# Optimization experiments

Measured on AMD Instinct MI355X. Metric: run time of the kernel, lower is better.

Reference implementation:

```python
import jax, jax.numpy as jnp
import numpy as np

H = 2048      # hidden_size
I = 768       # moe_intermediate_size
E = 32        # num_experts
K = 8         # num_experts_per_tok (top_k)
T = 1024      # tokens (batch * seq)


def setup_inputs() -> dict:
    key = jax.random.key(0)
    k1, k2, k3, k4 = jax.random.split(key, 4)
    return {
        "hidden_states": jax.random.normal(k1, (T, H), jnp.float32),
        "gate_weight": jax.random.normal(k2, (E, H), jnp.float32) * 0.02,
        "w13_weight": jax.random.normal(k3, (E, 2 * I, H), jnp.float32) * 0.02,
        "w2_weight": jax.random.normal(k4, (E, H, I), jnp.float32) * 0.02,
    }


def reference(hidden_states, gate_weight, w13_weight, w2_weight):
    x = hidden_states  # [T, H]
    # --- router (Qwen3MoeSparseMoeBlock gating) ---
    logits = x @ gate_weight.T                      # [T, E]
    probs = jax.nn.softmax(logits, axis=-1)
    topk_w, topk_idx = jax.lax.top_k(probs, K)      # [T, K]
    topk_w = topk_w / jnp.sum(topk_w, axis=-1, keepdims=True)  # norm_topk_prob
    # dense combine matrix [T, E]: routing weight per (token, expert), 0 if not selected
    combine = jnp.zeros((x.shape[0], E), x.dtype).at[
        jnp.arange(x.shape[0])[:, None], topk_idx
    ].add(topk_w)
    # --- expert FFNs (fused gate+up = w13, SiLU-gated, then w2 down-proj) ---
    h = jnp.einsum('th,eoh->eto', x, w13_weight)    # [E, T, 2I]
    gate, up = h[:, :, :I], h[:, :, I:]
    act = jax.nn.silu(gate) * up                    # [E, T, I]
    y = jnp.einsum('eti,ehi->eth', act, w2_weight)  # [E, T, H]
    # --- weighted combine ---
    return jnp.einsum('eth,te->th', y, combine)     # [T, H]
```

## Files before the change

kernel.cpp:

```cpp
#include <hip/hip_runtime.h>
#include <hip/hip_bf16.h>
#include <math.h>

#define T_TOK 1024
#define H_DIM 2048
#define I_DIM 768
#define E_NUM 32
#define K_TOP 8
#define BK 32
#define GRID_P 1024

typedef __bf16 bf16x8 __attribute__((ext_vector_type(8)));
typedef float  f32x4  __attribute__((ext_vector_type(4)));

__device__ __forceinline__ bf16x8 cvt2_bf16(const f32x4 a, const f32x4 b) {
    bf16x8 r;
    r[0] = (__bf16)a[0]; r[1] = (__bf16)a[1]; r[2] = (__bf16)a[2]; r[3] = (__bf16)a[3];
    r[4] = (__bf16)b[0]; r[5] = (__bf16)b[1]; r[6] = (__bf16)b[2]; r[7] = (__bf16)b[3];
    return r;
}

__device__ __forceinline__ int frag_off(int r, int kgrp8) {
    return (r >> 4) * 512 + kgrp8 * 128 + (r & 15) * 8;
}

__global__ __launch_bounds__(256) void router_kernel(
    const float* __restrict__ x, const float* __restrict__ gw,
    float* __restrict__ wdense, unsigned int* __restrict__ masks,
    __bf16* __restrict__ xb)
{
    const int t = blockIdx.x;
    const int tid = threadIdx.x;
    __shared__ float part[256];
    __shared__ float logits[E_NUM];

    {
        const float* xr2 = x + (size_t)t * H_DIM + tid * 8;
        const f32x4 a = *(const f32x4*)(xr2);
        const f32x4 b = *(const f32x4*)(xr2 + 4);
        *(bf16x8*)(xb + (size_t)t * H_DIM + tid * 8) = cvt2_bf16(a, b);
    }

    const int e = tid & 31;
    const int chunk = tid >> 5;
    const float* xr = x + (size_t)t * H_DIM;
    const float* gr = gw + (size_t)e * H_DIM;
    const int base = chunk * (H_DIM / 8);
    float s = 0.f;
    for (int h = 0; h < H_DIM / 8; h += 4) {
        const f32x4 xv = *reinterpret_cast<const f32x4*>(xr + base + h);
        const f32x4 gv = *reinterpret_cast<const f32x4*>(gr + base + h);
        s += xv[0]*gv[0] + xv[1]*gv[1] + xv[2]*gv[2] + xv[3]*gv[3];
    }
    part[tid] = s;
    __syncthreads();
    if (tid < E_NUM) {
        float tot = 0.f;
        for (int c = 0; c < 8; ++c) tot += part[c * 32 + tid];
        logits[tid] = tot;
    }
    __syncthreads();
    if (tid == 0) {
        float l[E_NUM];
        for (int i = 0; i < E_NUM; ++i) {
            l[i] = logits[i];
            wdense[(size_t)t * E_NUM + i] = 0.f;
        }
        unsigned mask = 0;
        int   idx[K_TOP];
        float lv[K_TOP];
        for (int k = 0; k < K_TOP; ++k) {
            float best = -1e30f; int bi = 0;
            for (int i = 0; i < E_NUM; ++i)
                if (!((mask >> i) & 1u) && l[i] > best) { best = l[i]; bi = i; }
            mask |= (1u << bi); idx[k] = bi; lv[k] = best;
        }
        const float m = lv[0];
        float den = 0.f;
        for (int k = 0; k < K_TOP; ++k) den += expf(lv[k] - m);
        for (int k = 0; k < K_TOP; ++k)
            wdense[(size_t)t * E_NUM + idx[k]] = expf(lv[k] - m) / den;
        masks[t] = mask;
    }
}

__global__ __launch_bounds__(1024) void route_kernel(
    const unsigned int* __restrict__ masks, const float* __restrict__ wdense,
    int* __restrict__ cnt, int* __restrict__ off, int* __restrict__ tbl,
    int* __restrict__ tok, float* __restrict__ wgt, int* __restrict__ posl)
{
    const int tid  = threadIdx.x;
    const int wv   = tid >> 6;
    const int lane = tid & 63;
    __shared__ int wcnt[E_NUM][16];
    __shared__ int woff[E_NUM][16];
    __shared__ int eoff[E_NUM];
    __shared__ int ecnt[E_NUM];

    const unsigned int m = masks[tid];
#pragma unroll
    for (int e = 0; e < E_NUM; ++e) {
        const unsigned long long b = __ballot((m >> e) & 1u);
        if (lane == 0) wcnt[e][wv] = __popcll(b);
    }
    __syncthreads();
    if (tid < E_NUM) {
        int r = 0;
        for (int w = 0; w < 16; ++w) { woff[tid][w] = r; r += wcnt[tid][w]; }
        ecnt[tid] = r;
    }
    __syncthreads();
    if (tid == 0) {
        int r = 0, nt = 0;
        for (int e = 0; e < E_NUM; ++e) {
            eoff[e] = r; off[e] = r;
            const int c = ecnt[e];
            cnt[e] = c;
            r += c;
            const int nz = (c + 127) >> 7;
            for (int z = 0; z < nz; ++z) tbl[1 + nt++] = (e << 8) | z;
        }
        tbl[0] = nt;
    }
    __syncthreads();
#pragma unroll
    for (int e = 0; e < E_NUM; ++e) {
        const int bit = (m >> e) & 1u;
        const unsigned long long b = __ballot(bit);
        if (bit) {
            const int pos = eoff[e] + woff[e][wv]
                          + (int)__popcll(b & ((1ULL << lane) - 1ULL));
            tok[pos] = tid;
            wgt[pos] = wdense[(size_t)tid * E_NUM + e];
            const int slot = __popc(m & ((1u << e) - 1u));
            posl[tid * K_TOP + slot] = pos;
        }
    }
}

#define GEMM_PHASE(P, Q)                                                       \
  {                                                                            \
    if (scur + 2 < NS) {                                                       \
      const int kk = (scur + 2) * BK;                                          \
      pa##P##_0 = *(const bf16x8*)(ap + kk);                                   \
      pa##P##_1 = *(const bf16x8*)(ap + kk + 8);                               \
      pb##P##_0 = *(const f32x4*)(wp + kk);                                    \
      pb##P##_1 = *(const f32x4*)(wp + kk + 4);                                \
      pb##P##_2 = *(const f32x4*)(wp + kk + 8);                                \
      pb##P##_3 = *(const f32x4*)(wp + kk + 12);                               \
    }                                                                          \
    bf16x8 af[4], bfr[4];                                                      \
    _Pragma("unroll")                                                          \
    for (int m = 0; m < 4; ++m)                                                \
      af[m] = *(const bf16x8*)&As[P][((wm >> 4) + m) * 512 + lane * 8];        \
    _Pragma("unroll")                                                          \
    for (int n = 0; n < 4; ++n)                                                \
      bfr[n] = *(const bf16x8*)&Bs[P][(wn * 4 + n) * 512 + lane * 8];          \
    __builtin_amdgcn_s_setprio(1);                                             \
    _Pragma("unroll")                                                          \
    for (int m = 0; m < 4; ++m)                                                \
      _Pragma("unroll")                                                        \
      for (int n = 0; n < 4; ++n)                                              \
        acc[m][n] = __builtin_amdgcn_mfma_f32_16x16x32_bf16(af[m], bfr[n],     \
                                                            acc[m][n], 0,0,0); \
    __builtin_amdgcn_s_setprio(0);                                             \
    if (scur + 1 < NS) {                                                       \
      *(bf16x8*)&As[Q][wo]       = pa##Q##_0;                                  \
      *(bf16x8*)&As[Q][wo + 128] = pa##Q##_1;                                  \
      *(bf16x8*)&Bs[Q][wo]       = cvt2_bf16(pb##Q##_0, pb##Q##_1);            \
      *(bf16x8*)&Bs[Q][wo + 128] = cvt2_bf16(pb##Q##_2, pb##Q##_3);            \
    }                                                                          \
    asm volatile("s_waitcnt lgkmcnt(0)" ::: "memory");                         \
    __builtin_amdgcn_s_barrier();                                              \
    ++scur;                                                                    \
  }

#define GEMM_PROLOGUE()                                                        \
    pa0_0 = *(const bf16x8*)(ap);                                              \
    pa0_1 = *(const bf16x8*)(ap + 8);                                          \
    pb0_0 = *(const f32x4*)(wp);                                               \
    pb0_1 = *(const f32x4*)(wp + 4);                                           \
    pb0_2 = *(const f32x4*)(wp + 8);                                           \
    pb0_3 = *(const f32x4*)(wp + 12);                                          \
    pa1_0 = *(const bf16x8*)(ap + BK);                                         \
    pa1_1 = *(const bf16x8*)(ap + BK + 8);                                     \
    pb1_0 = *(const f32x4*)(wp + BK);                                          \
    pb1_1 = *(const f32x4*)(wp + BK + 4);                                      \
    pb1_2 = *(const f32x4*)(wp + BK + 8);                                      \
    pb1_3 = *(const f32x4*)(wp + BK + 12);                                     \
    *(bf16x8*)&As[0][wo]       = pa0_0;                                        \
    *(bf16x8*)&As[0][wo + 128] = pa0_1;                                        \
    *(bf16x8*)&Bs[0][wo]       = cvt2_bf16(pb0_0, pb0_1);                      \
    *(bf16x8*)&Bs[0][wo + 128] = cvt2_bf16(pb0_2, pb0_3);                      \
    asm volatile("s_waitcnt lgkmcnt(0)" ::: "memory");                         \
    __builtin_amdgcn_s_barrier();

__global__ __launch_bounds__(256, 3) void gemm1_kernel(
    const __bf16* __restrict__ xb, const float* __restrict__ w13,
    const int* __restrict__ tok, const int* __restrict__ cnt,
    const int* __restrict__ off, const int* __restrict__ tbl,
    unsigned short* __restrict__ act)
{
    __shared__ __bf16 As[2][4096];
    __shared__ __bf16 Bs[2][4096];
    const int tid  = threadIdx.x;
    const int wid  = tid >> 6;
    const int lane = tid & 63;
    const int wm = (wid >> 1) * 64;
    const int wn = (wid & 1);
    const int lrow = lane & 15;
    const int sr = tid >> 1;
    const int kh = tid & 1;
    const int wo = frag_off(sr, kh * 2);
    const int NS = H_DIM / BK;

    const int W = tbl[0] * 12;
    for (int w = blockIdx.x; w < W; w += gridDim.x) {
        const int ti   = w / 12;
        const int nidx = w - ti * 12;
        const int ez = tbl[1 + ti];
        const int e  = ez >> 8;
        const int m0 = (ez & 255) * 128;
        const int c  = cnt[e];
        const int o  = off[e];
        const int n0 = nidx * 64;

        int rA = m0 + sr; rA = rA < c ? rA : c - 1;
        const __bf16* ap = xb + (size_t)tok[o + rA] * H_DIM + kh * 16;
        const int grp = sr >> 5;
        const int wrow = (grp & 1) * I_DIM + n0 + (grp >> 1) * 32 + (sr & 31);
        const float* wp = w13 + (size_t)e * (2 * I_DIM) * H_DIM
                              + (size_t)wrow * H_DIM + kh * 16;

        bf16x8 pa0_0, pa0_1, pa1_0, pa1_1;
        f32x4  pb0_0, pb0_1, pb0_2, pb0_3, pb1_0, pb1_1, pb1_2, pb1_3;
        f32x4  acc[4][4] = {};

        GEMM_PROLOGUE()

        int scur = 0;
        for (int it = 0; it < NS; it += 2) {
            GEMM_PHASE(0, 1)
            GEMM_PHASE(1, 0)
        }

#pragma unroll
        for (int m = 0; m < 4; ++m)
#pragma unroll
            for (int n = 0; n < 2; ++n)
#pragma unroll
                for (int i = 0; i < 4; ++i) {
                    const int row = m0 + wm + m * 16 + (lane >> 4) * 4 + i;
                    if (row < c) {
                        const int icol = n0 + wn * 32 + n * 16 + lrow;
                        const float g = acc[m][n][i];
                        const float u = acc[m][n + 2][i];
                        const float a = (g / (1.f + expf(-g))) * u;
                        act[(size_t)(o + row) * I_DIM + icol] =
                            __builtin_bit_cast(unsigned short, (__bf16)a);
                    }
                }
    }
}

__global__ __launch_bounds__(256, 3) void gemm2_kernel(
    const unsigned short* __restrict__ act, const float* __restrict__ w2,
    const int* __restrict__ tok, const float* __restrict__ wgt,
    const int* __restrict__ cnt, const int* __restrict__ off,
    const int* __restrict__ tbl, unsigned short* __restrict__ ybuf)
{
    __shared__ __bf16 As[2][4096];
    __shared__ __bf16 Bs[2][4096];
    const int tid  = threadIdx.x;
    const int wid  = tid >> 6;
    const int lane = tid & 63;
    const int wm = (wid >> 1) * 64;
    const int wn = (wid & 1);
    const int lrow = lane & 15;
    const int sr = tid >> 1;
    const int kh = tid & 1;
    const int wo = frag_off(sr, kh * 2);
    const int NS = I_DIM / BK;

    const int W = tbl[0] * 16;
    for (int w = blockIdx.x; w < W; w += gridDim.x) {
        const int ti   = w >> 4;
        const int nidx = w & 15;
        const int ez = tbl[1 + ti];
        const int e  = ez >> 8;
        const int m0 = (ez & 255) * 128;
        const int c  = cnt[e];
        const int o  = off[e];
        const int n0 = nidx * 128;

        int rA = m0 + sr; rA = rA < c ? rA : c - 1;
        const __bf16* ap = (const __bf16*)act + (size_t)(o + rA) * I_DIM + kh * 16;
        const float* wp = w2 + (size_t)e * H_DIM * I_DIM
                             + (size_t)(n0 + sr) * I_DIM + kh * 16;

        bf16x8 pa0_0, pa0_1, pa1_0, pa1_1;
        f32x4  pb0_0, pb0_1, pb0_2, pb0_3, pb1_0, pb1_1, pb1_2, pb1_3;
        f32x4  acc[4][4] = {};

        GEMM_PROLOGUE()

        int scur = 0;
        for (int it = 0; it < NS; it += 2) {
            GEMM_PHASE(0, 1)
            GEMM_PHASE(1, 0)
        }

#pragma unroll
        for (int m = 0; m < 4; ++m)
#pragma unroll
            for (int i = 0; i < 4; ++i) {
                const int row = m0 + wm + m * 16 + (lane >> 4) * 4 + i;
                if (row < c) {
                    const float wv = wgt[o + row];
                    unsigned short* yr = ybuf + (size_t)(o + row) * H_DIM
                                              + n0 + wn * 64 + lrow;
#pragma unroll
                    for (int n = 0; n < 4; ++n)
                        yr[n * 16] = __builtin_bit_cast(
                            unsigned short, (__bf16)(wv * acc[m][n][i]));
                }
            }
    }
}

__global__ __launch_bounds__(256) void combine_kernel(
    const unsigned short* __restrict__ ybuf, const int* __restrict__ posl,
    float* __restrict__ out)
{
    const int t = blockIdx.x;
    int p[K_TOP];
#pragma unroll
    for (int s = 0; s < K_TOP; ++s) p[s] = posl[t * K_TOP + s];
    const int h0 = threadIdx.x * 8;
    float a[8] = {};
#pragma unroll
    for (int s = 0; s < K_TOP; ++s) {
        const bf16x8 v = *(const bf16x8*)(ybuf + (size_t)p[s] * H_DIM + h0);
#pragma unroll
        for (int j = 0; j < 8; ++j) a[j] += (float)v[j];
    }
    f32x4 o0 = {a[0], a[1], a[2], a[3]};
    f32x4 o1 = {a[4], a[5], a[6], a[7]};
    *(f32x4*)(out + (size_t)t * H_DIM + h0)     = o0;
    *(f32x4*)(out + (size_t)t * H_DIM + h0 + 4) = o1;
}

extern "C" void kernel_launch(void* const* d_in, const int* in_sizes, int n_in,
                              void* d_out, int out_size, void* d_ws, size_t ws_size,
                              hipStream_t stream)
{
    const float* x   = (const float*)d_in[0];
    const float* gw  = (const float*)d_in[1];
    const float* w13 = (const float*)d_in[2];
    const float* w2  = (const float*)d_in[3];
    float* out = (float*)d_out;

    char* ws = (char*)d_ws;
    float*          wdense = (float*)(ws + 0x00000);
    unsigned int*   masks  = (unsigned int*)(ws + 0x20000);
    int*            cnt    = (int*)(ws + 0x21000);
    int*            off    = (int*)(ws + 0x21800);
    int*            tbl    = (int*)(ws + 0x22000);
    int*            tok    = (int*)(ws + 0x23000);
    float*          wgt    = (float*)(ws + 0x2B000);
    unsigned short* act    = (unsigned short*)(ws + 0x33000);
    __bf16*         xb     = (__bf16*)(ws + 0xC40000);
    int*            posl   = (int*)(ws + 0x1040000);
    unsigned short* ybuf   = (unsigned short*)(ws + 0x1100000);

    router_kernel<<<T_TOK, 256, 0, stream>>>(x, gw, wdense, masks, xb);
    route_kernel<<<1, 1024, 0, stream>>>(masks, wdense, cnt, off, tbl, tok, wgt, posl);
    gemm1_kernel<<<GRID_P, 256, 0, stream>>>(xb, w13, tok, cnt, off, tbl, act);
    gemm2_kernel<<<GRID_P, 256, 0, stream>>>(act, w2, tok, wgt, cnt, off, tbl, ybuf);
    combine_kernel<<<T_TOK, 256, 0, stream>>>(ybuf, posl, out);
}
```

Before: 337.7 us.

## Remap GEMM work items per XCD for weight-tile L2 reuse, stage router row in LDS

Both expert GEMM kernels now split the work list into eight contiguous slabs, one per XCD (chosen by blockIdx & 7), and order items n-tile-major so blocks on the same XCD share weight tiles and A rows through that XCD's L2. This targets cross-XCD duplication of fp32 weight reads. The router kernel stages the x row in shared memory instead of re-reading it from global memory, and the MFMA priority hints are removed. The slab scheme assumes the grid equals GRID_P, and the static split can leave some XCDs with uneven load.

```diff
diff --git a/kernel.cpp b/kernel.cpp
--- a/kernel.cpp
+++ b/kernel.cpp
@@ -31,6 +31,7 @@
 {
     const int t = blockIdx.x;
     const int tid = threadIdx.x;
+    __shared__ float xrow[H_DIM];
     __shared__ float part[256];
     __shared__ float logits[E_NUM];
 
@@ -38,18 +39,20 @@
         const float* xr2 = x + (size_t)t * H_DIM + tid * 8;
         const f32x4 a = *(const f32x4*)(xr2);
         const f32x4 b = *(const f32x4*)(xr2 + 4);
+        *(f32x4*)(xrow + tid * 8)     = a;
+        *(f32x4*)(xrow + tid * 8 + 4) = b;
         *(bf16x8*)(xb + (size_t)t * H_DIM + tid * 8) = cvt2_bf16(a, b);
     }
+    __syncthreads();
 
     const int e = tid & 31;
     const int chunk = tid >> 5;
-    const float* xr = x + (size_t)t * H_DIM;
     const float* gr = gw + (size_t)e * H_DIM;
     const int base = chunk * (H_DIM / 8);
     float s = 0.f;
     for (int h = 0; h < H_DIM / 8; h += 4) {
-        const f32x4 xv = *reinterpret_cast<const f32x4*>(xr + base + h);
-        const f32x4 gv = *reinterpret_cast<const f32x4*>(gr + base + h);
+        const f32x4 xv = *(const f32x4*)(xrow + base + h);
+        const f32x4 gv = *(const f32x4*)(gr + base + h);
         s += xv[0]*gv[0] + xv[1]*gv[1] + xv[2]*gv[2] + xv[3]*gv[3];
     }
     part[tid] = s;
@@ -156,14 +159,12 @@
     _Pragma("unroll")                                                          \
     for (int n = 0; n < 4; ++n)                                                \
       bfr[n] = *(const bf16x8*)&Bs[P][(wn * 4 + n) * 512 + lane * 8];          \
-    __builtin_amdgcn_s_setprio(1);                                             \
     _Pragma("unroll")                                                          \
     for (int m = 0; m < 4; ++m)                                                \
       _Pragma("unroll")                                                        \
       for (int n = 0; n < 4; ++n)                                              \
         acc[m][n] = __builtin_amdgcn_mfma_f32_16x16x32_bf16(af[m], bfr[n],     \
                                                             acc[m][n], 0,0,0); \
-    __builtin_amdgcn_s_setprio(0);                                             \
     if (scur + 1 < NS) {                                                       \
       *(bf16x8*)&As[Q][wo]       = pa##Q##_0;                                  \
       *(bf16x8*)&As[Q][wo + 128] = pa##Q##_1;                                  \
@@ -214,10 +215,16 @@
     const int wo = frag_off(sr, kh * 2);
     const int NS = H_DIM / BK;
 
-    const int W = tbl[0] * 12;
-    for (int w = blockIdx.x; w < W; w += gridDim.x) {
-        const int ti   = w / 12;
-        const int nidx = w - ti * 12;
+    const int NT = tbl[0];
+    const int W  = NT * 12;
+    const int slab = (W + 7) >> 3;
+    const int xcd  = blockIdx.x & 7;
+    const int jj   = blockIdx.x >> 3;
+    const int wlo  = xcd * slab;
+    const int whi  = (wlo + slab) < W ? (wlo + slab) : W;
+    for (int w = wlo + jj; w < whi; w += GRID_P / 8) {
+        const int nidx = w / NT;
+        const int ti   = w - nidx * NT;
         const int ez = tbl[1 + ti];
         const int e  = ez >> 8;
         const int m0 = (ez & 255) * 128;
@@ -282,10 +289,16 @@
     const int wo = frag_off(sr, kh * 2);
     const int NS = I_DIM / BK;
 
-    const int W = tbl[0] * 16;
-    for (int w = blockIdx.x; w < W; w += gridDim.x) {
-        const int ti   = w >> 4;
-        const int nidx = w & 15;
+    const int NT = tbl[0];
+    const int W  = NT * 16;
+    const int slab = (W + 7) >> 3;
+    const int xcd  = blockIdx.x & 7;
+    const int jj   = blockIdx.x >> 3;
+    const int wlo  = xcd * slab;
+    const int whi  = (wlo + slab) < W ? (wlo + slab) : W;
+    for (int w = wlo + jj; w < whi; w += GRID_P / 8) {
+        const int nidx = w / NT;
+        const int ti   = w - nidx * NT;
         const int ez = tbl[1 + ti];
         const int e  = ez >> 8;
         const int m0 = (ez & 255) * 128;
```

Measured after the change: 332.6 us, median of 2. About the same (-1.5%).

## Fuse both expert GEMMs into a persistent ticket-scheduled kernel with per-tile readiness flags

Applied to the files above, without the earlier changes.

Merges the gate/up GEMM and the down-projection GEMM into one persistent kernel. Blocks take work items from a global atomic ticket, and down-proj items spin-wait on a per-row-tile counter until all 12 gate/up tiles for that tile are written. The aim is to remove the launch gap and tail idle between the two GEMMs by letting them overlap. The router now stages the x row in shared memory instead of re-reading it from global memory, and the MFMA priority hints are dropped. The cost is an atomic grab per work item, spin waits, and a reliance on forward progress, which holds because tickets are taken in order.

```diff
diff --git a/kernel.cpp b/kernel.cpp
--- a/kernel.cpp
+++ b/kernel.cpp
@@ -31,6 +31,7 @@
 {
     const int t = blockIdx.x;
     const int tid = threadIdx.x;
+    __shared__ float xrow[H_DIM];
     __shared__ float part[256];
     __shared__ float logits[E_NUM];
 
@@ -38,18 +39,20 @@
         const float* xr2 = x + (size_t)t * H_DIM + tid * 8;
         const f32x4 a = *(const f32x4*)(xr2);
         const f32x4 b = *(const f32x4*)(xr2 + 4);
+        *(f32x4*)(xrow + tid * 8)     = a;
+        *(f32x4*)(xrow + tid * 8 + 4) = b;
         *(bf16x8*)(xb + (size_t)t * H_DIM + tid * 8) = cvt2_bf16(a, b);
     }
+    __syncthreads();
 
     const int e = tid & 31;
     const int chunk = tid >> 5;
-    const float* xr = x + (size_t)t * H_DIM;
     const float* gr = gw + (size_t)e * H_DIM;
     const int base = chunk * (H_DIM / 8);
     float s = 0.f;
     for (int h = 0; h < H_DIM / 8; h += 4) {
-        const f32x4 xv = *reinterpret_cast<const f32x4*>(xr + base + h);
-        const f32x4 gv = *reinterpret_cast<const f32x4*>(gr + base + h);
+        const f32x4 xv = *(const f32x4*)(xrow + base + h);
+        const f32x4 gv = *(const f32x4*)(gr + base + h);
         s += xv[0]*gv[0] + xv[1]*gv[1] + xv[2]*gv[2] + xv[3]*gv[3];
     }
     part[tid] = s;
@@ -87,7 +90,8 @@
 __global__ __launch_bounds__(1024) void route_kernel(
     const unsigned int* __restrict__ masks, const float* __restrict__ wdense,
     int* __restrict__ cnt, int* __restrict__ off, int* __restrict__ tbl,
-    int* __restrict__ tok, float* __restrict__ wgt, int* __restrict__ posl)
+    int* __restrict__ tok, float* __restrict__ wgt, int* __restrict__ posl,
+    int* __restrict__ ticket, int* __restrict__ rdy)
 {
     const int tid  = threadIdx.x;
     const int wv   = tid >> 6;
@@ -96,6 +100,9 @@
     __shared__ int woff[E_NUM][16];
     __shared__ int eoff[E_NUM];
     __shared__ int ecnt[E_NUM];
+
+    if (tid == 0) *ticket = 0;
+    if (tid < 128) rdy[tid] = 0;
 
     const unsigned int m = masks[tid];
 #pragma unroll
@@ -156,14 +163,12 @@
     _Pragma("unroll")                                                          \
     for (int n = 0; n < 4; ++n)                                                \
       bfr[n] = *(const bf16x8*)&Bs[P][(wn * 4 + n) * 512 + lane * 8];          \
-    __builtin_amdgcn_s_setprio(1);                                             \
     _Pragma("unroll")                                                          \
     for (int m = 0; m < 4; ++m)                                                \
       _Pragma("unroll")                                                        \
       for (int n = 0; n < 4; ++n)                                              \
         acc[m][n] = __builtin_amdgcn_mfma_f32_16x16x32_bf16(af[m], bfr[n],     \
                                                             acc[m][n], 0,0,0); \
-    __builtin_amdgcn_s_setprio(0);                                             \
     if (scur + 1 < NS) {                                                       \
       *(bf16x8*)&As[Q][wo]       = pa##Q##_0;                                  \
       *(bf16x8*)&As[Q][wo + 128] = pa##Q##_1;                                  \
@@ -195,14 +200,17 @@
     asm volatile("s_waitcnt lgkmcnt(0)" ::: "memory");                         \
     __builtin_amdgcn_s_barrier();
 
-__global__ __launch_bounds__(256, 3) void gemm1_kernel(
+__global__ __launch_bounds__(256, 3) void moe_kernel(
     const __bf16* __restrict__ xb, const float* __restrict__ w13,
-    const int* __restrict__ tok, const int* __restrict__ cnt,
+    const float* __restrict__ w2, const int* __restrict__ tok,
+    const float* __restrict__ wgt, const int* __restrict__ cnt,
     const int* __restrict__ off, const int* __restrict__ tbl,
-    unsigned short* __restrict__ act)
+    unsigned short* act, unsigned short* __restrict__ ybuf,
+    int* ticket, int* rdy)
 {
     __shared__ __bf16 As[2][4096];
     __shared__ __bf16 Bs[2][4096];
+    __shared__ int curw;
     const int tid  = threadIdx.x;
     const int wid  = tid >> 6;
     const int lane = tid & 63;
@@ -212,119 +220,121 @@
     const int sr = tid >> 1;
     const int kh = tid & 1;
     const int wo = frag_off(sr, kh * 2);
-    const int NS = H_DIM / BK;
-
-    const int W = tbl[0] * 12;
-    for (int w = blockIdx.x; w < W; w += gridDim.x) {
-        const int ti   = w / 12;
-        const int nidx = w - ti * 12;
-        const int ez = tbl[1 + ti];
-        const int e  = ez >> 8;
-        const int m0 = (ez & 255) * 128;
-        const int c  = cnt[e];
-        const int o  = off[e];
-        const int n0 = nidx * 64;
-
-        int rA = m0 + sr; rA = rA < c ? rA : c - 1;
-        const __bf16* ap = xb + (size_t)tok[o + rA] * H_DIM + kh * 16;
-        const int grp = sr >> 5;
-        const int wrow = (grp & 1) * I_DIM + n0 + (grp >> 1) * 32 + (sr & 31);
-        const float* wp = w13 + (size_t)e * (2 * I_DIM) * H_DIM
-                              + (size_t)wrow * H_DIM + kh * 16;
-
-        bf16x8 pa0_0, pa0_1, pa1_0, pa1_1;
-        f32x4  pb0_0, pb0_1, pb0_2, pb0_3, pb1_0, pb1_1, pb1_2, pb1_3;
-        f32x4  acc[4][4] = {};
-
-        GEMM_PROLOGUE()
-
-        int scur = 0;
-        for (int it = 0; it < NS; it += 2) {
-            GEMM_PHASE(0, 1)
-            GEMM_PHASE(1, 0)
-        }
-
-#pragma unroll
-        for (int m = 0; m < 4; ++m)
-#pragma unroll
-            for (int n = 0; n < 2; ++n)
+
+    const int NT = tbl[0];
+    const int W1 = NT * 12;
+    const int W2 = NT * 16;
+
+    for (;;) {
+        __syncthreads();
+        if (tid == 0) curw = atomicAdd(ticket, 1);
+        __syncthreads();
+        const int w = curw;
+        if (w >= W1 + W2) break;
+
+        if (w < W1) {
+            const int ti   = w / 12;
+            const int nidx = w - ti * 12;
+            const int ez = tbl[1 + ti];
+            const int e  = ez >> 8;
+            const int m0 = (ez & 255) * 128;
+            const int c  = cnt[e];
+            const int o  = off[e];
+            const int n0 = nidx * 64;
+            const int NS = H_DIM / BK;
+
+            int rA = m0 + sr; rA = rA < c ? rA : c - 1;
+            const __bf16* ap = xb + (size_t)tok[o + rA] * H_DIM + kh * 16;
+            const int grp = sr >> 5;
+            const int wrow = (grp & 1) * I_DIM + n0 + (grp >> 1) * 32 + (sr & 31);
+            const float* wp = w13 + (size_t)e * (2 * I_DIM) * H_DIM
+                                  + (size_t)wrow * H_DIM + kh * 16;
+
+            bf16x8 pa0_0, pa0_1, pa1_0, pa1_1;
+            f32x4  pb0_0, pb0_1, pb0_2, pb0_3, pb1_0, pb1_1, pb1_2, pb1_3;
+            f32x4  acc[4][4] = {};
+
+            GEMM_PROLOGUE()
+
+            int scur = 0;
+            for (int it = 0; it < NS; it += 2) {
+                GEMM_PHASE(0, 1)
+                GEMM_PHASE(1, 0)
+            }
+
+#pragma unroll
+            for (int m = 0; m < 4; ++m)
+#pragma unroll
+                for (int n = 0; n < 2; ++n)
+#pragma unroll
+                    for (int i = 0; i < 4; ++i) {
+                        const int row = m0 + wm + m * 16 + (lane >> 4) * 4 + i;
+                        if (row < c) {
+                            const int icol = n0 + wn * 32 + n * 16 + lrow;
+                            const float g = acc[m][n][i];
+                            const float u = acc[m][n + 2][i];
+                            const float a = (g / (1.f + expf(-g))) * u;
+                            act[(size_t)(o + row) * I_DIM + icol] =
+                                __builtin_bit_cast(unsigned short, (__bf16)a);
+                        }
+                    }
+
+            __threadfence();
+            __syncthreads();
+            if (tid == 0) atomicAdd(&rdy[ti], 1);
+        } else {
+            const int w2i  = w - W1;
+            const int ti   = w2i >> 4;
+            const int nidx = w2i & 15;
+            const int ez = tbl[1 + ti];
+            const int e  = ez >> 8;
+            const int m0 = (ez & 255) * 128;
+            const int c  = cnt[e];
+            const int o  = off[e];
+            const int n0 = nidx * 128;
+            const int NS = I_DIM / BK;
+
+            if (tid == 0) {
+                while (__hip_atomic_load(&rdy[ti], __ATOMIC_ACQUIRE,
+                                         __HIP_MEMORY_SCOPE_AGENT) < 12)
+                    __builtin_amdgcn_s_sleep(2);
+            }
+            __syncthreads();
+            __threadfence();
+
+            int rA = m0 + sr; rA = rA < c ? rA : c - 1;
+            const __bf16* ap = (const __bf16*)act + (size_t)(o + rA) * I_DIM + kh * 16;
+            const float* wp = w2 + (size_t)e * H_DIM * I_DIM
+                                 + (size_t)(n0 + sr) * I_DIM + kh * 16;
+
+            bf16x8 pa0_0, pa0_1, pa1_0, pa1_1;
+            f32x4  pb0_0, pb0_1, pb0_2, pb0_3, pb1_0, pb1_1, pb1_2, pb1_3;
+            f32x4  acc[4][4] = {};
+
+            GEMM_PROLOGUE()
+
+            int scur = 0;
+            for (int it = 0; it < NS; it += 2) {
+                GEMM_PHASE(0, 1)
+                GEMM_PHASE(1, 0)
+            }
+
+#pragma unroll
+            for (int m = 0; m < 4; ++m)
 #pragma unroll
                 for (int i = 0; i < 4; ++i) {
                     const int row = m0 + wm + m * 16 + (lane >> 4) * 4 + i;
                     if (row < c) {
-                        const int icol = n0 + wn * 32 + n * 16 + lrow;
-                        const float g = acc[m][n][i];
-                        const float u = acc[m][n + 2][i];
-                        const float a = (g / (1.f + expf(-g))) * u;
-                        act[(size_t)(o + row) * I_DIM + icol] =
-                            __builtin_bit_cast(unsigned short, (__bf16)a);
+                        const float wv = wgt[o + row];
+                        unsigned short* yr = ybuf + (size_t)(o + row) * H_DIM
+                                                  + n0 + wn * 64 + lrow;
+#pragma unroll
+                        for (int n = 0; n < 4; ++n)
+                            yr[n * 16] = __builtin_bit_cast(
+                                unsigned short, (__bf16)(wv * acc[m][n][i]));
                     }
                 }
-    }
-}
-
-__global__ __launch_bounds__(256, 3) void gemm2_kernel(
-    const unsigned short* __restrict__ act, const float* __restrict__ w2,
-    const int* __restrict__ tok, const float* __restrict__ wgt,
-    const int* __restrict__ cnt, const int* __restrict__ off,
-    const int* __restrict__ tbl, unsigned short* __restrict__ ybuf)
-{
-    __shared__ __bf16 As[2][4096];
-    __shared__ __bf16 Bs[2][4096];
-    const int tid  = threadIdx.x;
-    const int wid  = tid >> 6;
-    const int lane = tid & 63;
-    const int wm = (wid >> 1) * 64;
-    const int wn = (wid & 1);
-    const int lrow = lane & 15;
-    const int sr = tid >> 1;
-    const int kh = tid & 1;
-    const int wo = frag_off(sr, kh * 2);
-    const int NS = I_DIM / BK;
-
-    const int W = tbl[0] * 16;
-    for (int w = blockIdx.x; w < W; w += gridDim.x) {
-        const int ti   = w >> 4;
-        const int nidx = w & 15;
-        const int ez = tbl[1 + ti];
-        const int e  = ez >> 8;
-        const int m0 = (ez & 255) * 128;
-        const int c  = cnt[e];
-        const int o  = off[e];
-        const int n0 = nidx * 128;
-
-        int rA = m0 + sr; rA = rA < c ? rA : c - 1;
-        const __bf16* ap = (const __bf16*)act + (size_t)(o + rA) * I_DIM + kh * 16;
-        const float* wp = w2 + (size_t)e * H_DIM * I_DIM
-                             + (size_t)(n0 + sr) * I_DIM + kh * 16;
-
-        bf16x8 pa0_0, pa0_1, pa1_0, pa1_1;
-        f32x4  pb0_0, pb0_1, pb0_2, pb0_3, pb1_0, pb1_1, pb1_2, pb1_3;
-        f32x4  acc[4][4] = {};
-
-        GEMM_PROLOGUE()
-
-        int scur = 0;
-        for (int it = 0; it < NS; it += 2) {
-            GEMM_PHASE(0, 1)
-            GEMM_PHASE(1, 0)
-        }
-
-#pragma unroll
-        for (int m = 0; m < 4; ++m)
-#pragma unroll
-            for (int i = 0; i < 4; ++i) {
-                const int row = m0 + wm + m * 16 + (lane >> 4) * 4 + i;
-                if (row < c) {
-                    const float wv = wgt[o + row];
-                    unsigned short* yr = ybuf + (size_t)(o + row) * H_DIM
-                                              + n0 + wn * 64 + lrow;
-#pragma unroll
-                    for (int n = 0; n < 4; ++n)
-                        yr[n * 16] = __builtin_bit_cast(
-                            unsigned short, (__bf16)(wv * acc[m][n][i]));
-                }
-            }
+        }
     }
 }
 
@@ -365,6 +375,8 @@
     unsigned int*   masks  = (unsigned int*)(ws + 0x20000);
     int*            cnt    = (int*)(ws + 0x21000);
     int*            off    = (int*)(ws + 0x21800);
+    int*            ticket = (int*)(ws + 0x21900);
+    int*            rdy    = (int*)(ws + 0x21A00);
     int*            tbl    = (int*)(ws + 0x22000);
     int*            tok    = (int*)(ws + 0x23000);
     float*          wgt    = (float*)(ws + 0x2B000);
@@ -374,8 +386,9 @@
     unsigned short* ybuf   = (unsigned short*)(ws + 0x1100000);
 
     router_kernel<<<T_TOK, 256, 0, stream>>>(x, gw, wdense, masks, xb);
-    route_kernel<<<1, 1024, 0, stream>>>(masks, wdense, cnt, off, tbl, tok, wgt, posl);
-    gemm1_kernel<<<GRID_P, 256, 0, stream>>>(xb, w13, tok, cnt, off, tbl, act);
-    gemm2_kernel<<<GRID_P, 256, 0, stream>>>(act, w2, tok, wgt, cnt, off, tbl, ybuf);
+    route_kernel<<<1, 1024, 0, stream>>>(masks, wdense, cnt, off, tbl, tok,
+                                         wgt, posl, ticket, rdy);
+    moe_kernel<<<GRID_P, 256, 0, stream>>>(xb, w13, w2, tok, wgt, cnt, off,
+                                           tbl, act, ybuf, ticket, rdy);
     combine_kernel<<<T_TOK, 256, 0, stream>>>(ybuf, posl, out);
 }
```

Measured after the change: 849.8 us. 2.52x slower.
